# Kernel tuning notes

Measured on AMD Instinct MI355X. Metric: run time of the kernel, lower is better.

The kernel has to match this reference:

```python
import jax, jax.numpy as jnp
import numpy as np


def setup_inputs() -> dict:
    key = jax.random.key(0)
    k1, k2 = jax.random.split(key)
    B, T, F, H = 64, 512, 512, 1024
    x = jax.random.normal(k1, (B, T, F), dtype=jnp.float32)
    W = jax.random.normal(k2, (F + H, H), dtype=jnp.float32) * (1.0 / np.sqrt(F + H))
    b = jnp.zeros((H,), dtype=jnp.float32)
    return {"x": x, "W": W, "b": b}


def reference(x, W, b):
    # Vanilla tanh RNN: state_t = tanh([x_t, state_{t-1}] @ W + b); return last state.
    B, T, F = x.shape
    H = b.shape[0]
    Wx, Wh = W[:F], W[F:]  # split weight: input part [F,H], recurrent part [H,H]
    # Precompute input projections for all timesteps in one big GEMM.
    xproj = jnp.einsum('btf,fh->bth', x, Wx) + b  # [B,T,H]

    def step(state, xp_t):
        state = jnp.tanh(xp_t + state @ Wh)
        return state, None

    state0 = jnp.zeros((B, H), dtype=x.dtype)
    final_state, _ = jax.lax.scan(step, state0, jnp.swapaxes(xproj, 0, 1))
    return final_state
```

## Files before the change

kernel.cpp:

```cpp
#include <hip/hip_runtime.h>


typedef _Float16 f16;
typedef _Float16 f16x8 __attribute__((ext_vector_type(8)));
typedef _Float16 f16x4 __attribute__((ext_vector_type(4)));
typedef float f32x4 __attribute__((ext_vector_type(4)));

#define B_  64
#define T_  512
#define F_  512
#define H_  1024

#define XPH_OFF  0ull
#define WXT_OFF  67108864ull
#define WHT_OFF  68157440ull
#define SBUF_OFF 70254592ull
#define BAR_OFF  70516736ull
#define WS_NEED  70518784ull

__global__ __launch_bounds__(256) void k_prep(const float* __restrict__ W,
                                              f16* __restrict__ WxT,
                                              f16* __restrict__ WhT) {
  __shared__ float tile[32][33];
  const int tid = threadIdx.x;
  const int kt = blockIdx.x >> 5;
  const int ht = blockIdx.x & 31;
#pragma unroll
  for (int p = 0; p < 4; ++p) {
    int kr = p * 8 + (tid >> 5);
    tile[kr][tid & 31] = W[(size_t)(kt * 32 + kr) * 1024 + ht * 32 + (tid & 31)];
  }
  __syncthreads();
  const int hl = tid >> 3;
  const int kq = tid & 7;
  f16x4 v;
#pragma unroll
  for (int j = 0; j < 4; ++j) v[j] = (f16)tile[kq * 4 + j][hl];
  const int h = ht * 32 + hl;
  const int kg = kt * 32 + kq * 4;
  if (kg < 512) *(f16x4*)(WxT + (size_t)h * 512 + kg) = v;
  else          *(f16x4*)(WhT + (size_t)h * 1024 + (kg - 512)) = v;
}

__global__ __launch_bounds__(256) void k_xproj(const float* __restrict__ x,
                                               const f16* __restrict__ WxT,
                                               const float* __restrict__ bias,
                                               f16* __restrict__ xph) {
  __shared__ __align__(16) unsigned char Al[65536];
  __shared__ __align__(16) unsigned char Bl[65536];
  const int tid = threadIdx.x;
  const int l = tid & 63, w = tid >> 6;
  const int lane15 = l & 15, sub = l >> 4;
  const int m0 = blockIdx.x * 64;
  const int bidx = m0 >> 9;
  const int t0 = m0 & 511;

  {
    const int r = tid >> 2, qq = tid & 3;
    const float* xs = x + (size_t)(m0 + r) * 512;
#pragma unroll
    for (int i = 0; i < 16; ++i) {
      int s = qq * 16 + i;
      int c = s ^ (r & 7);
      const float4 f0 = *(const float4*)(xs + c * 8);
      const float4 f1 = *(const float4*)(xs + c * 8 + 4);
      f16x8 v;
      v[0] = (f16)f0.x; v[1] = (f16)f0.y; v[2] = (f16)f0.z; v[3] = (f16)f0.w;
      v[4] = (f16)f1.x; v[5] = (f16)f1.y; v[6] = (f16)f1.z; v[7] = (f16)f1.w;
      *(f16x8*)(Al + r * 1024 + s * 16) = v;
    }
  }

  const int mh = (w >> 1) * 32, nh = (w & 1) * 32;
  const int rA0 = mh + lane15, rA1 = mh + 16 + lane15;
  const int rB0 = nh + lane15, rB1 = nh + 16 + lane15;

  for (int nb = 0; nb < 16; ++nb) {
    const int n0 = nb * 64;
    __syncthreads();
    {
      const int r = tid >> 2, qq = tid & 3;
      const f16* bs = WxT + (size_t)(n0 + r) * 512;
#pragma unroll
      for (int i = 0; i < 16; ++i) {
        int s = qq * 16 + i;
        int c = s ^ (r & 7);
        f16x8 v = *(const f16x8*)(bs + c * 8);
        *(f16x8*)(Bl + r * 1024 + s * 16) = v;
      }
    }
    __syncthreads();
    f32x4 acc00 = {0.f,0.f,0.f,0.f}, acc01 = {0.f,0.f,0.f,0.f};
    f32x4 acc10 = {0.f,0.f,0.f,0.f}, acc11 = {0.f,0.f,0.f,0.f};
#pragma unroll
    for (int kk = 0; kk < 16; ++kk) {
      const int s = kk * 4 + sub;
      f16x8 a0 = *(const f16x8*)(Al + rA0 * 1024 + ((s ^ (rA0 & 7)) << 4));
      f16x8 a1 = *(const f16x8*)(Al + rA1 * 1024 + ((s ^ (rA1 & 7)) << 4));
      f16x8 b0 = *(const f16x8*)(Bl + rB0 * 1024 + ((s ^ (rB0 & 7)) << 4));
      f16x8 b1 = *(const f16x8*)(Bl + rB1 * 1024 + ((s ^ (rB1 & 7)) << 4));
      acc00 = __builtin_amdgcn_mfma_f32_16x16x32_f16(a0, b0, acc00, 0, 0, 0);
      acc01 = __builtin_amdgcn_mfma_f32_16x16x32_f16(a0, b1, acc01, 0, 0, 0);
      acc10 = __builtin_amdgcn_mfma_f32_16x16x32_f16(a1, b0, acc10, 0, 0, 0);
      acc11 = __builtin_amdgcn_mfma_f32_16x16x32_f16(a1, b1, acc11, 0, 0, 0);
    }
    const float bv0 = bias[n0 + nh + lane15];
    const float bv1 = bias[n0 + nh + 16 + lane15];
#pragma unroll
    for (int j = 0; j < 4; ++j) {
      const int r0 = mh + sub * 4 + j;
      const int r1 = mh + 16 + sub * 4 + j;
      const size_t row0 = (size_t)(t0 + r0) * 64 + bidx;
      const size_t row1 = (size_t)(t0 + r1) * 64 + bidx;
      xph[row0 * 1024 + n0 + nh + lane15]      = (f16)(acc00[j] + bv0);
      xph[row0 * 1024 + n0 + nh + 16 + lane15] = (f16)(acc01[j] + bv1);
      xph[row1 * 1024 + n0 + nh + lane15]      = (f16)(acc10[j] + bv0);
      xph[row1 * 1024 + n0 + nh + 16 + lane15] = (f16)(acc11[j] + bv1);
    }
  }
}

__global__ __launch_bounds__(256) void k_rnn(const f16* __restrict__ xph,
                                             const f16* __restrict__ WhT,
                                             f16* sbuf, unsigned* bar,
                                             float* __restrict__ out) {
  __shared__ __align__(16) unsigned char lds[131072];
  unsigned char* WhL = lds;
  unsigned char* stL = lds + 98304;
  const int tid = threadIdx.x;
  const int l = tid & 63, w = tid >> 6;
  const int lane15 = l & 15, sub = l >> 4;
  const int bid = blockIdx.x;
  const int group = (bid & 7) >> 1;
  const int slice = (bid >> 3) * 2 + (bid & 1);

  for (int i = 0; i < 24; ++i) {
    int s = i * 256 + tid;
    int r = s / 96;
    int ks = 32 + (s - r * 96);
    f16x8 v = *(const f16x8*)(WhT + (size_t)(slice * 64 + r) * 1024 + ks * 8);
    *(f16x8*)(WhL + r * 1536 + ((ks ^ (r & 7)) - 32) * 16) = v;
  }
  const int colL = slice * 64 + w * 16 + lane15;
  f16x8 breg[8];
  {
    const f16* src = WhT + (size_t)colL * 1024 + sub * 8;
#pragma unroll
    for (int kk = 0; kk < 8; ++kk) breg[kk] = *(const f16x8*)(src + kk * 32);
  }
  const int rA = lane15, xA = rA & 7;
  const int rB = w * 16 + lane15, xB = rB & 7;
  const unsigned char* stLb = stL + rA * 2048;
  const unsigned char* whb  = WhL + rB * 1536;
  unsigned* barg = bar + group * 128;

  for (int t = 0; t < T_; ++t) {
    const char* ib = (const char*)sbuf + (size_t)(t & 1) * 131072 + group * 32768;
    char*       ob = (char*)sbuf + (size_t)((t + 1) & 1) * 131072 + group * 32768;

    float xpv[4];
#pragma unroll
    for (int j = 0; j < 4; ++j)
      xpv[j] = (float)xph[(size_t)(t * 64 + group * 16 + sub * 4 + j) * 1024 + colL];

    unsigned long long tmp[16];
#pragma unroll
    for (int i = 0; i < 16; ++i)
      tmp[i] = __hip_atomic_load((const unsigned long long*)(ib + i * 2048 + tid * 8),
                                 __ATOMIC_RELAXED, __HIP_MEMORY_SCOPE_AGENT);
#pragma unroll
    for (int i = 0; i < 16; ++i)
      *(unsigned long long*)(stL + i * 2048 + tid * 8) = tmp[i];
    __syncthreads();

    f32x4 acc0 = {0.f,0.f,0.f,0.f}, acc1 = {0.f,0.f,0.f,0.f};
#pragma unroll
    for (int kk = 0; kk < 32; ++kk) {
      const int s = kk * 4 + sub;
      f16x8 a = *(const f16x8*)(stLb + ((s ^ xA) << 4));
      f16x8 b = (kk < 8) ? breg[kk]
                         : *(const f16x8*)(whb + (((s ^ xB) - 32) << 4));
      if (kk & 1) acc1 = __builtin_amdgcn_mfma_f32_16x16x32_f16(a, b, acc1, 0, 0, 0);
      else        acc0 = __builtin_amdgcn_mfma_f32_16x16x32_f16(a, b, acc0, 0, 0, 0);
    }

    if (t == T_ - 1) {
#pragma unroll
      for (int j = 0; j < 4; ++j) {
        const int r = sub * 4 + j;
        out[(size_t)(group * 16 + r) * 1024 + colL] =
            tanhf(acc0[j] + acc1[j] + xpv[j]);
      }
      break;
    }
#pragma unroll
    for (int j = 0; j < 4; ++j) {
      const int r = sub * 4 + j;
      f16 hv = (f16)tanhf(acc0[j] + acc1[j] + xpv[j]);
      const int byteoff = r * 2048 + (((colL >> 3) ^ (r & 7)) << 4) + (colL & 7) * 2;
      unsigned short bits;
      __builtin_memcpy(&bits, &hv, 2);
      __hip_atomic_store((unsigned short*)(ob + byteoff), bits,
                         __ATOMIC_RELAXED, __HIP_MEMORY_SCOPE_AGENT);
    }
    __syncthreads();
    if (tid == 0) {
      asm volatile("s_waitcnt vmcnt(0)" ::: "memory");
      __hip_atomic_fetch_add(barg, 1u, __ATOMIC_RELAXED, __HIP_MEMORY_SCOPE_AGENT);
      const unsigned tgt = 16u * (unsigned)(t + 1);
      while (__hip_atomic_load(barg, __ATOMIC_RELAXED, __HIP_MEMORY_SCOPE_AGENT) < tgt) {}
    }
    __syncthreads();
  }
}

extern "C" void kernel_launch(void* const* d_in, const int* in_sizes, int n_in,
                              void* d_out, int out_size, void* d_ws, size_t ws_size,
                              hipStream_t stream) {
  const float* x    = (const float*)d_in[0];
  const float* W    = (const float*)d_in[1];
  const float* bias = (const float*)d_in[2];
  float* out = (float*)d_out;
  char* w = (char*)d_ws;

  f16* xph = (f16*)(w + XPH_OFF);
  f16* WxT = (f16*)(w + WXT_OFF);
  f16* WhT = (f16*)(w + WHT_OFF);
  f16* sbuf = (f16*)(w + SBUF_OFF);
  unsigned* bar = (unsigned*)(w + BAR_OFF);

  hipMemsetAsync(w + SBUF_OFF, 0, 262144 + 2048, stream);

  k_prep<<<dim3(48 * 32), dim3(256), 0, stream>>>(W, WxT, WhT);
  k_xproj<<<dim3(512), dim3(256), 0, stream>>>(x, WxT, bias, xph);
  k_rnn<<<dim3(64), dim3(256), 0, stream>>>(xph, WhT, sbuf, bar, out);
}
```

Baseline: 1.769 ms.

## Replace counter barrier with per-block flags, keep Wh in registers, pack state stores

The recurrent kernel now holds its whole Wh column slice in registers (32 f16x8 per lane) and no longer stages it in LDS. The per-group atomic counter barrier is replaced by per-producer flags: each block publishes a step counter, and each 16-thread subgroup waits only on the flag of the slice it is about to read before loading that slice. Hidden-state outputs are transposed through a small LDS tile so each thread writes one packed 8-byte store instead of four 2-byte atomics, and the MFMA chain is split across four accumulators. Costs are much higher register pressure, possible spills, and a dependence on the correctness of the relaxed-ordering flag protocol.

```diff
diff --git a/kernel.cpp b/kernel.cpp
--- a/kernel.cpp
+++ b/kernel.cpp
@@ -120,13 +120,13 @@
   }
 }
 
-__global__ __launch_bounds__(256) void k_rnn(const f16* __restrict__ xph,
-                                             const f16* __restrict__ WhT,
-                                             f16* sbuf, unsigned* bar,
-                                             float* __restrict__ out) {
-  __shared__ __align__(16) unsigned char lds[131072];
-  unsigned char* WhL = lds;
-  unsigned char* stL = lds + 98304;
+__global__ __launch_bounds__(256, 1) void k_rnn(const f16* __restrict__ xph,
+                                                const f16* __restrict__ WhT,
+                                                f16* sbuf, unsigned* bar,
+                                                float* __restrict__ out) {
+  __shared__ __align__(16) unsigned char lds[32768 + 2176];
+  unsigned char* stL  = lds;
+  unsigned char* tbuf = lds + 32768;
   const int tid = threadIdx.x;
   const int l = tid & 63, w = tid >> 6;
   const int lane15 = l & 15, sub = l >> 4;
@@ -134,25 +134,20 @@
   const int group = (bid & 7) >> 1;
   const int slice = (bid >> 3) * 2 + (bid & 1);
 
-  for (int i = 0; i < 24; ++i) {
-    int s = i * 256 + tid;
-    int r = s / 96;
-    int ks = 32 + (s - r * 96);
-    f16x8 v = *(const f16x8*)(WhT + (size_t)(slice * 64 + r) * 1024 + ks * 8);
-    *(f16x8*)(WhL + r * 1536 + ((ks ^ (r & 7)) - 32) * 16) = v;
-  }
   const int colL = slice * 64 + w * 16 + lane15;
-  f16x8 breg[8];
+  f16x8 breg[32];
   {
     const f16* src = WhT + (size_t)colL * 1024 + sub * 8;
 #pragma unroll
-    for (int kk = 0; kk < 8; ++kk) breg[kk] = *(const f16x8*)(src + kk * 32);
+    for (int kk = 0; kk < 32; ++kk) breg[kk] = *(const f16x8*)(src + kk * 32);
   }
   const int rA = lane15, xA = rA & 7;
-  const int rB = w * 16 + lane15, xB = rB & 7;
   const unsigned char* stLb = stL + rA * 2048;
-  const unsigned char* whb  = WhL + rB * 1536;
-  unsigned* barg = bar + group * 128;
+
+  const int p = tid >> 4, q = tid & 15;
+  unsigned* myflag   = bar + (group * 16 + slice) * 8;
+  unsigned* pollflag = bar + (group * 16 + p) * 8;
+  const bool do_poll = (p != slice);
 
   for (int t = 0; t < T_; ++t) {
     const char* ib = (const char*)sbuf + (size_t)(t & 1) * 131072 + group * 32768;
@@ -163,54 +158,67 @@
     for (int j = 0; j < 4; ++j)
       xpv[j] = (float)xph[(size_t)(t * 64 + group * 16 + sub * 4 + j) * 1024 + colL];
 
-    unsigned long long tmp[16];
-#pragma unroll
-    for (int i = 0; i < 16; ++i)
-      tmp[i] = __hip_atomic_load((const unsigned long long*)(ib + i * 2048 + tid * 8),
-                                 __ATOMIC_RELAXED, __HIP_MEMORY_SCOPE_AGENT);
-#pragma unroll
-    for (int i = 0; i < 16; ++i)
-      *(unsigned long long*)(stL + i * 2048 + tid * 8) = tmp[i];
+    if (t > 0 && do_poll) {
+      while (__hip_atomic_load(pollflag, __ATOMIC_RELAXED,
+                               __HIP_MEMORY_SCOPE_AGENT) < (unsigned)t) {}
+    }
+    {
+      unsigned long long tmp[16];
+      const char* src = ib + p * 128 + q * 8;
+#pragma unroll
+      for (int i = 0; i < 16; ++i)
+        tmp[i] = __hip_atomic_load((const unsigned long long*)(src + i * 2048),
+                                   __ATOMIC_RELAXED, __HIP_MEMORY_SCOPE_AGENT);
+#pragma unroll
+      for (int i = 0; i < 16; ++i)
+        *(unsigned long long*)(stL + i * 2048 + p * 128 + q * 8) = tmp[i];
+    }
     __syncthreads();
 
     f32x4 acc0 = {0.f,0.f,0.f,0.f}, acc1 = {0.f,0.f,0.f,0.f};
-#pragma unroll
-    for (int kk = 0; kk < 32; ++kk) {
-      const int s = kk * 4 + sub;
-      f16x8 a = *(const f16x8*)(stLb + ((s ^ xA) << 4));
-      f16x8 b = (kk < 8) ? breg[kk]
-                         : *(const f16x8*)(whb + (((s ^ xB) - 32) << 4));
-      if (kk & 1) acc1 = __builtin_amdgcn_mfma_f32_16x16x32_f16(a, b, acc1, 0, 0, 0);
-      else        acc0 = __builtin_amdgcn_mfma_f32_16x16x32_f16(a, b, acc0, 0, 0, 0);
-    }
+    f32x4 acc2 = {0.f,0.f,0.f,0.f}, acc3 = {0.f,0.f,0.f,0.f};
+#pragma unroll
+    for (int kk = 0; kk < 32; kk += 4) {
+      f16x8 a0 = *(const f16x8*)(stLb + ((((kk + 0) * 4 + sub) ^ xA) << 4));
+      f16x8 a1 = *(const f16x8*)(stLb + ((((kk + 1) * 4 + sub) ^ xA) << 4));
+      f16x8 a2 = *(const f16x8*)(stLb + ((((kk + 2) * 4 + sub) ^ xA) << 4));
+      f16x8 a3 = *(const f16x8*)(stLb + ((((kk + 3) * 4 + sub) ^ xA) << 4));
+      acc0 = __builtin_amdgcn_mfma_f32_16x16x32_f16(a0, breg[kk + 0], acc0, 0, 0, 0);
+      acc1 = __builtin_amdgcn_mfma_f32_16x16x32_f16(a1, breg[kk + 1], acc1, 0, 0, 0);
+      acc2 = __builtin_amdgcn_mfma_f32_16x16x32_f16(a2, breg[kk + 2], acc2, 0, 0, 0);
+      acc3 = __builtin_amdgcn_mfma_f32_16x16x32_f16(a3, breg[kk + 3], acc3, 0, 0, 0);
+    }
+    float rv[4];
+#pragma unroll
+    for (int j = 0; j < 4; ++j)
+      rv[j] = acc0[j] + acc1[j] + acc2[j] + acc3[j] + xpv[j];
 
     if (t == T_ - 1) {
 #pragma unroll
-      for (int j = 0; j < 4; ++j) {
-        const int r = sub * 4 + j;
-        out[(size_t)(group * 16 + r) * 1024 + colL] =
-            tanhf(acc0[j] + acc1[j] + xpv[j]);
-      }
+      for (int j = 0; j < 4; ++j)
+        out[(size_t)(group * 16 + sub * 4 + j) * 1024 + colL] = tanhf(rv[j]);
       break;
     }
+
 #pragma unroll
     for (int j = 0; j < 4; ++j) {
-      const int r = sub * 4 + j;
-      f16 hv = (f16)tanhf(acc0[j] + acc1[j] + xpv[j]);
-      const int byteoff = r * 2048 + (((colL >> 3) ^ (r & 7)) << 4) + (colL & 7) * 2;
-      unsigned short bits;
-      __builtin_memcpy(&bits, &hv, 2);
-      __hip_atomic_store((unsigned short*)(ob + byteoff), bits,
+      f16 hv = (f16)tanhf(rv[j]);
+      *(f16*)(tbuf + (sub * 4 + j) * 136 + (w * 16 + lane15) * 2) = hv;
+    }
+    asm volatile("s_waitcnt lgkmcnt(0)" ::: "memory");
+    const int rr = lane15, cg = sub;
+    unsigned long long packed =
+        *(const unsigned long long*)(tbuf + rr * 136 + (w * 16 + cg * 4) * 2);
+    const int c0 = slice * 64 + w * 16 + cg * 4;
+    const int byteoff = rr * 2048 + (((c0 >> 3) ^ (rr & 7)) << 4) + (c0 & 7) * 2;
+    __hip_atomic_store((unsigned long long*)(ob + byteoff), packed,
+                       __ATOMIC_RELAXED, __HIP_MEMORY_SCOPE_AGENT);
+
+    asm volatile("s_waitcnt vmcnt(0)" ::: "memory");
+    __syncthreads();
+    if (tid == 0)
+      __hip_atomic_store(myflag, (unsigned)(t + 1),
                          __ATOMIC_RELAXED, __HIP_MEMORY_SCOPE_AGENT);
-    }
-    __syncthreads();
-    if (tid == 0) {
-      asm volatile("s_waitcnt vmcnt(0)" ::: "memory");
-      __hip_atomic_fetch_add(barg, 1u, __ATOMIC_RELAXED, __HIP_MEMORY_SCOPE_AGENT);
-      const unsigned tgt = 16u * (unsigned)(t + 1);
-      while (__hip_atomic_load(barg, __ATOMIC_RELAXED, __HIP_MEMORY_SCOPE_AGENT) < tgt) {}
-    }
-    __syncthreads();
   }
 }
 
```

Measured after the change: 1.808 ms. 1.02x slower.

## Replace atomic counter barrier with parity-bit tagged state exchange between blocks

Applied to the files above, without the earlier changes.

Removes the per-step global atomic counter barrier. Each 8-byte chunk of the exchanged hidden state now carries a phase bit in its lowest mantissa bit, and consumers spin-reload the chunks until every parity bit matches the expected phase. Outputs are first staged through LDS so each thread stores one packed 64-bit word instead of four 16-bit atomic stores, and a small init kernel replaces the memset. This cuts the barrier round-trip latency on the serial recurrence path, at the cost of corrupting one low bit of the f16 state and of data-bit polling correctness subtleties.

```diff
diff --git a/kernel.cpp b/kernel.cpp
--- a/kernel.cpp
+++ b/kernel.cpp
@@ -5,6 +5,8 @@
 typedef _Float16 f16x8 __attribute__((ext_vector_type(8)));
 typedef _Float16 f16x4 __attribute__((ext_vector_type(4)));
 typedef float f32x4 __attribute__((ext_vector_type(4)));
+typedef unsigned long long u64;
+typedef unsigned u32;
 
 #define B_  64
 #define T_  512
@@ -15,8 +17,15 @@
 #define WXT_OFF  67108864ull
 #define WHT_OFF  68157440ull
 #define SBUF_OFF 70254592ull
-#define BAR_OFF  70516736ull
-#define WS_NEED  70518784ull
+#define WS_NEED  70516736ull
+
+#define ALD64(p)    __hip_atomic_load((const u64*)(p), __ATOMIC_RELAXED, __HIP_MEMORY_SCOPE_AGENT)
+#define AST64(p, v) __hip_atomic_store((u64*)(p), (v), __ATOMIC_RELAXED, __HIP_MEMORY_SCOPE_AGENT)
+
+__global__ __launch_bounds__(256) void k_init(u64* __restrict__ sbuf) {
+  const unsigned i = blockIdx.x * 256 + threadIdx.x;
+  sbuf[i] = (i >= 16384) ? 1ull : 0ull;
+}
 
 __global__ __launch_bounds__(256) void k_prep(const float* __restrict__ W,
                                               f16* __restrict__ WxT,
@@ -120,13 +129,14 @@
   }
 }
 
-__global__ __launch_bounds__(256) void k_rnn(const f16* __restrict__ xph,
-                                             const f16* __restrict__ WhT,
-                                             f16* sbuf, unsigned* bar,
-                                             float* __restrict__ out) {
-  __shared__ __align__(16) unsigned char lds[131072];
-  unsigned char* WhL = lds;
-  unsigned char* stL = lds + 98304;
+__global__ __launch_bounds__(256, 1) void k_rnn(const f16* __restrict__ xph,
+                                                const f16* __restrict__ WhT,
+                                                f16* sbuf,
+                                                float* __restrict__ out) {
+  __shared__ __align__(16) unsigned char lds[131072 + 2176];
+  unsigned char* WhL  = lds;
+  unsigned char* stL  = lds + 98304;
+  unsigned char* tbuf = lds + 131072;
   const int tid = threadIdx.x;
   const int l = tid & 63, w = tid >> 6;
   const int lane15 = l & 15, sub = l >> 4;
@@ -152,7 +162,10 @@
   const int rB = w * 16 + lane15, xB = rB & 7;
   const unsigned char* stLb = stL + rA * 2048;
   const unsigned char* whb  = WhL + rB * 1536;
-  unsigned* barg = bar + group * 128;
+
+  const int p = tid >> 4, q = tid & 15;
+  const int c0s = slice * 64 + w * 16 + sub * 4;
+  const int stoff = lane15 * 2048 + (((c0s >> 3) ^ (lane15 & 7)) << 4) + (c0s & 7) * 2;
 
   for (int t = 0; t < T_; ++t) {
     const char* ib = (const char*)sbuf + (size_t)(t & 1) * 131072 + group * 32768;
@@ -163,14 +176,24 @@
     for (int j = 0; j < 4; ++j)
       xpv[j] = (float)xph[(size_t)(t * 64 + group * 16 + sub * 4 + j) * 1024 + colL];
 
-    unsigned long long tmp[16];
-#pragma unroll
-    for (int i = 0; i < 16; ++i)
-      tmp[i] = __hip_atomic_load((const unsigned long long*)(ib + i * 2048 + tid * 8),
-                                 __ATOMIC_RELAXED, __HIP_MEMORY_SCOPE_AGENT);
-#pragma unroll
-    for (int i = 0; i < 16; ++i)
-      *(unsigned long long*)(stL + i * 2048 + tid * 8) = tmp[i];
+    {
+      u64 tmp[16];
+      const char* src = ib + p * 128 + q * 8;
+#pragma unroll
+      for (int i = 0; i < 16; ++i) tmp[i] = ALD64(src + i * 2048);
+      const u32 want = (u32)((t >> 1) & 1);
+      for (;;) {
+        u32 bad = 0;
+#pragma unroll
+        for (int i = 0; i < 16; ++i) bad |= ((u32)tmp[i] ^ want) & 1u;
+        if (bad == 0) break;
+#pragma unroll
+        for (int i = 0; i < 16; ++i) tmp[i] = ALD64(src + i * 2048);
+      }
+#pragma unroll
+      for (int i = 0; i < 16; ++i)
+        *(u64*)(stL + i * 2048 + p * 128 + q * 8) = tmp[i];
+    }
     __syncthreads();
 
     f32x4 acc0 = {0.f,0.f,0.f,0.f}, acc1 = {0.f,0.f,0.f,0.f};
@@ -193,22 +216,17 @@
       }
       break;
     }
+
 #pragma unroll
     for (int j = 0; j < 4; ++j) {
-      const int r = sub * 4 + j;
       f16 hv = (f16)tanhf(acc0[j] + acc1[j] + xpv[j]);
-      const int byteoff = r * 2048 + (((colL >> 3) ^ (r & 7)) << 4) + (colL & 7) * 2;
-      unsigned short bits;
-      __builtin_memcpy(&bits, &hv, 2);
-      __hip_atomic_store((unsigned short*)(ob + byteoff), bits,
-                         __ATOMIC_RELAXED, __HIP_MEMORY_SCOPE_AGENT);
-    }
-    __syncthreads();
-    if (tid == 0) {
-      asm volatile("s_waitcnt vmcnt(0)" ::: "memory");
-      __hip_atomic_fetch_add(barg, 1u, __ATOMIC_RELAXED, __HIP_MEMORY_SCOPE_AGENT);
-      const unsigned tgt = 16u * (unsigned)(t + 1);
-      while (__hip_atomic_load(barg, __ATOMIC_RELAXED, __HIP_MEMORY_SCOPE_AGENT) < tgt) {}
+      *(f16*)(tbuf + (sub * 4 + j) * 136 + (w * 16 + lane15) * 2) = hv;
+    }
+    asm volatile("s_waitcnt lgkmcnt(0)" ::: "memory");
+    {
+      u64 packed = *(const u64*)(tbuf + lane15 * 136 + (w * 16 + sub * 4) * 2);
+      packed = (packed & ~1ull) | (u64)(((t + 1) >> 1) & 1);
+      AST64(ob + stoff, packed);
     }
     __syncthreads();
   }
@@ -227,11 +245,10 @@
   f16* WxT = (f16*)(w + WXT_OFF);
   f16* WhT = (f16*)(w + WHT_OFF);
   f16* sbuf = (f16*)(w + SBUF_OFF);
-  unsigned* bar = (unsigned*)(w + BAR_OFF);
-
-  hipMemsetAsync(w + SBUF_OFF, 0, 262144 + 2048, stream);
+
+  k_init<<<dim3(128), dim3(256), 0, stream>>>((u64*)(w + SBUF_OFF));
 
   k_prep<<<dim3(48 * 32), dim3(256), 0, stream>>>(W, WxT, WhT);
   k_xproj<<<dim3(512), dim3(256), 0, stream>>>(x, WxT, bias, xph);
-  k_rnn<<<dim3(64), dim3(256), 0, stream>>>(xph, WhT, sbuf, bar, out);
-}
+  k_rnn<<<dim3(64), dim3(256), 0, stream>>>(xph, WhT, sbuf, out);
+}
```

New measurement: 1.775 ms. No clear change (+0.3%).
